# Performance work log

Hardware: AMD Instinct MI355X
Metric: run time of the kernel (lower is better)

Reference implementation:

```python
import jax, jax.numpy as jnp
import numpy as np

OUT_DIM = 64
NUM_HEADS = 8
HID = NUM_HEADS * OUT_DIM  # 512
ALPHA = 0.01  # leaky relu slope
N_NODES = 20000
N_EDGES = 100000
MP_LEN = 3


def setup_inputs() -> dict:
    key = jax.random.key(0)
    ks = jax.random.split(key, 8)
    s = 1.0 / np.sqrt(HID)
    return {
        "features": jax.random.normal(ks[0], (N_NODES, OUT_DIM), jnp.float32),
        "W_ih": jax.random.normal(ks[1], (3 * HID, OUT_DIM), jnp.float32) * s,
        "W_hh": jax.random.normal(ks[2], (3 * HID, HID), jnp.float32) * s,
        "b_ih": jax.random.normal(ks[3], (3 * HID,), jnp.float32) * s,
        "b_hh": jax.random.normal(ks[4], (3 * HID,), jnp.float32) * s,
        "attn": jax.random.normal(ks[5], (NUM_HEADS, OUT_DIM), jnp.float32) * 0.1,
        "edge_metapath_indices": jax.random.randint(ks[6], (N_EDGES, MP_LEN), 0, N_NODES),
        "edge_dst": jax.random.randint(ks[7], (N_EDGES,), 0, N_NODES),
    }


def _gru_last_hidden(x_seq, W_ih, W_hh, b_ih, b_hh):
    """x_seq: [L, E, D] -> final hidden [E, HID] (torch nn.GRU math, h0=0)."""
    E = x_seq.shape[1]
    h0 = jnp.zeros((E, HID), x_seq.dtype)

    def step(h, x):
        gi = x @ W_ih.T + b_ih  # [E, 3*HID]
        gh = h @ W_hh.T + b_hh  # [E, 3*HID]
        i_r, i_z, i_n = jnp.split(gi, 3, axis=-1)
        h_r, h_z, h_n = jnp.split(gh, 3, axis=-1)
        r = jax.nn.sigmoid(i_r + h_r)
        z = jax.nn.sigmoid(i_z + h_z)
        n = jnp.tanh(i_n + r * h_n)
        h_new = (1.0 - z) * n + z * h
        return h_new, None

    h_last, _ = jax.lax.scan(step, h0, x_seq)
    return h_last


def reference(features, W_ih, W_hh, b_ih, b_hh, attn,
              edge_metapath_indices, edge_dst):
    N = features.shape[0]
    # gather metapath node features: [E, L, D] -> GRU over L
    edata = features[edge_metapath_indices]
    h = _gru_last_hidden(jnp.transpose(edata, (1, 0, 2)), W_ih, W_hh, b_ih, b_hh)
    eft = h.reshape(-1, NUM_HEADS, OUT_DIM)  # [E, H, D]
    # attention logits per edge/head + leaky relu
    a = jnp.sum(eft * attn[None], axis=-1)  # [E, H]
    a = jnp.where(a >= 0, a, ALPHA * a)
    # edge softmax grouped by destination node
    amax = jax.ops.segment_max(a, edge_dst, num_segments=N)  # [N, H]
    ea = jnp.exp(a - amax[edge_dst])
    denom = jax.ops.segment_sum(ea, edge_dst, num_segments=N)  # [N, H]
    alpha = ea / denom[edge_dst]  # [E, H]
    # weighted message aggregation (sum) to destination nodes
    msg = eft * alpha[:, :, None]  # [E, H, D]
    ret = jax.ops.segment_sum(msg, edge_dst, num_segments=N)  # [N, H, D]
    return ret
```

## Files before the change

kernel.cpp:

```cpp
#include <hip/hip_runtime.h>
#include <hip/hip_bf16.h>

#define N_NODES 20000
#define N_EDGES 100000
#define HID 512
#define G3 1536
#define NH 8
#define OD 64

typedef __hip_bfloat16 bf16;
typedef __attribute__((ext_vector_type(8))) short bf16x8;
typedef __attribute__((ext_vector_type(4))) float f32x4;

__device__ __forceinline__ float fsig(float x) { return 1.0f / (1.0f + __expf(-x)); }
__device__ __forceinline__ float ftanh(float x) { return 1.0f - 2.0f / (__expf(2.0f * x) + 1.0f); }
__device__ __forceinline__ float b2f(bf16 b) { return __bfloat162float(b); }
__device__ __forceinline__ bf16 f2b(float f) { return __float2bfloat16(f); }
__device__ __forceinline__ float bs2f(short s) {
    return __uint_as_float(((unsigned)(unsigned short)s) << 16);
}
__device__ __forceinline__ float us2f(unsigned short s) {
    return __uint_as_float(((unsigned)s) << 16);
}
__device__ __forceinline__ short f2bs(float f) {
    bf16 b = __float2bfloat16(f);
    return *reinterpret_cast<short*>(&b);
}
__device__ __forceinline__ unsigned ford(float f) {
    unsigned u = __float_as_uint(f);
    return (u & 0x80000000u) ? ~u : (u | 0x80000000u);
}
__device__ __forceinline__ float iford(unsigned u) {
    return __uint_as_float((u & 0x80000000u) ? (u & 0x7fffffffu) : ~u);
}

__device__ __forceinline__ void g2l16(const void* g, void* l) {
#if __has_builtin(__builtin_amdgcn_global_load_lds)
    __builtin_amdgcn_global_load_lds((const __attribute__((address_space(1))) char*)g,
                                     (__attribute__((address_space(3))) char*)l, 16, 0, 0);
#else
    *(bf16x8*)l = *(const bf16x8*)g;
#endif
}


__global__ __launch_bounds__(256) void k_prep(const float* __restrict__ Whh,
                                              const float* __restrict__ Wih,
                                              bf16* __restrict__ WTs,
                                              float* __restrict__ WIT) {
    int t = blockIdx.x * 256 + threadIdx.x;
    if (t < 98304) {
        int T = t >> 10, c = (t >> 6) & 15, l = t & 63;
        int n = T * 16 + (l & 15);
        int k = c * 32 + ((l >> 4) << 3);
        const float* src = Whh + (size_t)n * 512 + k;
        bf16x8 v;
#pragma unroll
        for (int j = 0; j < 8; ++j) v[j] = f2bs(src[j]);
        *(bf16x8*)(WTs + (size_t)t * 8) = v;
    } else {
        int u = t - 98304;
        int d = u / 1536, j = u % 1536;
        WIT[u] = Wih[(size_t)j * 64 + d];
    }
}

__global__ __launch_bounds__(256) void k_count(const int* __restrict__ dst,
                                               unsigned* __restrict__ cnt) {
    int e = blockIdx.x * 256 + threadIdx.x;
    if (e < N_EDGES) atomicAdd(&cnt[dst[e]], 1u);
}

#define SCAN_CH 79
__global__ __launch_bounds__(256) void k_scan(const unsigned* __restrict__ cnt,
                                              unsigned* __restrict__ base,
                                              unsigned* __restrict__ cursor) {
    __shared__ unsigned ls[256];
    int t = threadIdx.x;
    int s0 = t * SCAN_CH;
    int s1 = s0 + SCAN_CH < N_NODES ? s0 + SCAN_CH : N_NODES;
    unsigned s = 0;
    for (int i = s0; i < s1; ++i) s += cnt[i];
    ls[t] = s;
    __syncthreads();
    for (int d = 1; d < 256; d <<= 1) {
        unsigned v = (t >= d) ? ls[t - d] : 0u;
        __syncthreads();
        ls[t] += v;
        __syncthreads();
    }
    unsigned run = ls[t] - s;
    for (int i = s0; i < s1; ++i) {
        base[i] = run; cursor[i] = run; run += cnt[i];
    }
    if (t == 255) base[N_NODES] = ls[255];
}

__global__ __launch_bounds__(256) void k_fill(const int* __restrict__ dst,
                                              unsigned* __restrict__ cursor,
                                              unsigned* __restrict__ csr) {
    int e = blockIdx.x * 256 + threadIdx.x;
    if (e < N_EDGES) {
        unsigned p = atomicAdd(&cursor[dst[e]], 1u);
        csr[p] = (unsigned)e;
    }
}

__global__ __launch_bounds__(256) void k_gi(const float* __restrict__ feat,
                                            const float* __restrict__ WIT,
                                            const float* __restrict__ b_ih,
                                            const float* __restrict__ b_hh,
                                            bf16* __restrict__ G,
                                            bf16* __restrict__ H1) {
    __shared__ float fs[16][64];
    const int n0 = blockIdx.x * 16;
    const int k = blockIdx.y * 256 + threadIdx.x;
    for (int i = threadIdx.x; i < 16 * 64; i += 256)
        fs[0][i] = feat[(size_t)n0 * 64 + i];
    __syncthreads();
    float acc[3][16];
#pragma unroll
    for (int g = 0; g < 3; ++g) {
        float b = b_ih[g * 512 + k];
#pragma unroll
        for (int e = 0; e < 16; ++e) acc[g][e] = b;
    }
    for (int d = 0; d < 64; d += 4) {
        float w[3][4];
#pragma unroll
        for (int u = 0; u < 4; ++u)
#pragma unroll
            for (int g = 0; g < 3; ++g)
                w[g][u] = WIT[(size_t)(d + u) * G3 + g * 512 + k];
#pragma unroll
        for (int e = 0; e < 16; ++e) {
            float4 f = *(const float4*)&fs[e][d];
#pragma unroll
            for (int g = 0; g < 3; ++g)
                acc[g][e] += w[g][0] * f.x + w[g][1] * f.y + w[g][2] * f.z + w[g][3] * f.w;
        }
    }
    const float br = b_hh[k], bz = b_hh[512 + k], bn = b_hh[1024 + k];
#pragma unroll
    for (int e = 0; e < 16; ++e) {
        bf16* dst = G + (size_t)(n0 + e) * G3 + k * 3;
        dst[0] = f2b(acc[0][e]);
        dst[1] = f2b(acc[1][e]);
        dst[2] = f2b(acc[2][e]);
        float r1 = fsig(acc[0][e] + br);
        float z1 = fsig(acc[1][e] + bz);
        float n1 = ftanh(acc[2][e] + r1 * bn);
        H1[(size_t)(n0 + e) * HID + k] = f2b((1.0f - z1) * n1);
    }
}

__global__ __launch_bounds__(256, 2) void k_gh2(const bf16* __restrict__ H1,
                                                const bf16* __restrict__ WTs,
                                                const float* __restrict__ b_hh,
                                                bf16* __restrict__ GH2) {
    __shared__ short Bs[3 * 8192];
    const int tid = threadIdx.x;
    const int wave = tid >> 6, lane = tid & 63;
    const int m0 = blockIdx.x * 128;
    const int k0 = (lane >> 4) << 3;

    bf16x8 afrag[2][16];
#pragma unroll
    for (int t = 0; t < 2; ++t) {
        int row = m0 + wave * 32 + t * 16 + (lane & 15);
        int ar = row < N_NODES ? row : N_NODES - 1;
#pragma unroll
        for (int c = 0; c < 16; ++c)
            afrag[t][c] = *(const bf16x8*)(H1 + (size_t)ar * HID + c * 32 + k0);
    }

    const bf16* wp[12];
    short* lp[12];
#pragma unroll
    for (int i = 0; i < 12; ++i) {
        int p = tid + i * 256;
        int g = p >> 10, q = p & 1023;
        wp[i] = WTs + (size_t)g * 32 * 8192 + q * 8;
        lp[i] = &Bs[g * 8192 + q * 8];
    }

    const int col = lane & 15;
    const int qb = (lane >> 4) << 2;
    for (int jt = 0; jt < 32; ++jt) {
        __syncthreads();
#pragma unroll
        for (int i = 0; i < 12; ++i) {
            g2l16(wp[i], lp[i]);
            wp[i] += 8192;
        }
        __syncthreads();
        f32x4 acc[2][3];
#pragma unroll
        for (int t = 0; t < 2; ++t)
#pragma unroll
            for (int g = 0; g < 3; ++g) acc[t][g] = (f32x4){0, 0, 0, 0};
        const int boff = lane * 8;
#pragma unroll
        for (int c = 0; c < 16; ++c) {
            bf16x8 b0 = *(const bf16x8*)&Bs[0 * 8192 + c * 512 + boff];
            bf16x8 b1 = *(const bf16x8*)&Bs[1 * 8192 + c * 512 + boff];
            bf16x8 b2 = *(const bf16x8*)&Bs[2 * 8192 + c * 512 + boff];
#pragma unroll
            for (int t = 0; t < 2; ++t) {
                acc[t][0] = __builtin_amdgcn_mfma_f32_16x16x32_bf16(afrag[t][c], b0, acc[t][0], 0, 0, 0);
                acc[t][1] = __builtin_amdgcn_mfma_f32_16x16x32_bf16(afrag[t][c], b1, acc[t][1], 0, 0, 0);
                acc[t][2] = __builtin_amdgcn_mfma_f32_16x16x32_bf16(afrag[t][c], b2, acc[t][2], 0, 0, 0);
            }
        }
        const int cj = jt * 16 + col;
        const float br = b_hh[cj], bz = b_hh[512 + cj], bn = b_hh[1024 + cj];
#pragma unroll
        for (int t = 0; t < 2; ++t)
#pragma unroll
            for (int q = 0; q < 4; ++q) {
                int e = m0 + wave * 32 + t * 16 + qb + q;
                if (e < N_NODES) {
                    bf16* dst = GH2 + (size_t)e * G3 + cj * 3;
                    dst[0] = f2b(acc[t][0][q] + br);
                    dst[1] = f2b(acc[t][1][q] + bz);
                    dst[2] = f2b(acc[t][2][q] + bn);
                }
            }
    }
}

__global__ __launch_bounds__(256) void k_h2(const bf16* __restrict__ G,
                                            const bf16* __restrict__ GH2,
                                            const bf16* __restrict__ H1,
                                            const int* __restrict__ emi,
                                            bf16* __restrict__ h2) {
    size_t i = (size_t)blockIdx.x * 256 + threadIdx.x;
    int e = (int)(i >> 6);
    int kc = (int)(i & 63) * 8;
    int i0 = emi[(size_t)e * 3 + 0];
    int i1 = emi[(size_t)e * 3 + 1];
    const bf16* g1p = G + (size_t)i1 * G3 + kc * 3;
    const bf16* ghp = GH2 + (size_t)i0 * G3 + kc * 3;
    bf16x8 h1v = *(const bf16x8*)(H1 + (size_t)i0 * HID + kc);
    short s1[24], sh[24];
    {
        bf16x8 a0 = *(const bf16x8*)g1p, a1 = *(const bf16x8*)(g1p + 8), a2 = *(const bf16x8*)(g1p + 16);
        bf16x8 c0 = *(const bf16x8*)ghp, c1 = *(const bf16x8*)(ghp + 8), c2 = *(const bf16x8*)(ghp + 16);
#pragma unroll
        for (int j = 0; j < 8; ++j) {
            s1[j] = a0[j]; s1[8 + j] = a1[j]; s1[16 + j] = a2[j];
            sh[j] = c0[j]; sh[8 + j] = c1[j]; sh[16 + j] = c2[j];
        }
    }
    bf16x8 out;
#pragma unroll
    for (int j = 0; j < 8; ++j) {
        float r = fsig(bs2f(s1[j * 3 + 0]) + bs2f(sh[j * 3 + 0]));
        float z = fsig(bs2f(s1[j * 3 + 1]) + bs2f(sh[j * 3 + 1]));
        float n = ftanh(bs2f(s1[j * 3 + 2]) + r * bs2f(sh[j * 3 + 2]));
        out[j] = f2bs((1.0f - z) * n + z * bs2f(h1v[j]));
    }
    *(bf16x8*)(h2 + (size_t)e * HID + kc) = out;
}

__global__ __launch_bounds__(256, 2) void k_gemm3(const bf16* __restrict__ G,
                                                  const bf16* __restrict__ WTs,
                                                  const float* __restrict__ b_hh,
                                                  const int* __restrict__ emi,
                                                  bf16* __restrict__ h2) {
    __shared__ short Bs[3 * 8192];
    __shared__ int si2[128];
    const int tid = threadIdx.x;
    const int wave = tid >> 6, lane = tid & 63;
    const int m0 = blockIdx.x * 128;
    if (tid < 128) {
        int e = m0 + tid;
        si2[tid] = emi[(size_t)(e < N_EDGES ? e : N_EDGES - 1) * 3 + 2];
    }
    const int k0 = (lane >> 4) << 3;

    bf16x8 afrag[2][16];
#pragma unroll
    for (int t = 0; t < 2; ++t) {
        int row = m0 + wave * 32 + t * 16 + (lane & 15);
        int ar = row < N_EDGES ? row : N_EDGES - 1;
#pragma unroll
        for (int c = 0; c < 16; ++c)
            afrag[t][c] = *(const bf16x8*)(h2 + (size_t)ar * HID + c * 32 + k0);
    }

    const bf16* wp[12];
    short* lp[12];
#pragma unroll
    for (int i = 0; i < 12; ++i) {
        int p = tid + i * 256;
        int g = p >> 10, q = p & 1023;
        wp[i] = WTs + (size_t)g * 32 * 8192 + q * 8;
        lp[i] = &Bs[g * 8192 + q * 8];
    }

    const int col = lane & 15;
    const int qb = (lane >> 4) << 2;
    for (int jt = 0; jt < 32; ++jt) {
        __syncthreads();
#pragma unroll
        for (int i = 0; i < 12; ++i) {
            g2l16(wp[i], lp[i]);
            wp[i] += 8192;
        }
        const int cj = jt * 16 + col;
        const float br = b_hh[cj], bz = b_hh[512 + cj], bn = b_hh[1024 + cj];
        unsigned short pg[2][4][3], ph[2][4];
#pragma unroll
        for (int t = 0; t < 2; ++t)
#pragma unroll
            for (int q = 0; q < 4; ++q) {
                int li = wave * 32 + t * 16 + qb + q;
                int e = m0 + li;
                int ec = e < N_EDGES ? e : N_EDGES - 1;
                const unsigned short* g2p =
                    (const unsigned short*)(G + (size_t)si2[li] * G3 + cj * 3);
                pg[t][q][0] = g2p[0]; pg[t][q][1] = g2p[1]; pg[t][q][2] = g2p[2];
                ph[t][q] = ((const unsigned short*)h2)[(size_t)ec * HID + cj];
            }
        __syncthreads();
        f32x4 acc[2][3];
#pragma unroll
        for (int t = 0; t < 2; ++t)
#pragma unroll
            for (int g = 0; g < 3; ++g) acc[t][g] = (f32x4){0, 0, 0, 0};
        const int boff = lane * 8;
#pragma unroll
        for (int c = 0; c < 16; ++c) {
            bf16x8 b0 = *(const bf16x8*)&Bs[0 * 8192 + c * 512 + boff];
            bf16x8 b1 = *(const bf16x8*)&Bs[1 * 8192 + c * 512 + boff];
            bf16x8 b2 = *(const bf16x8*)&Bs[2 * 8192 + c * 512 + boff];
#pragma unroll
            for (int t = 0; t < 2; ++t) {
                acc[t][0] = __builtin_amdgcn_mfma_f32_16x16x32_bf16(afrag[t][c], b0, acc[t][0], 0, 0, 0);
                acc[t][1] = __builtin_amdgcn_mfma_f32_16x16x32_bf16(afrag[t][c], b1, acc[t][1], 0, 0, 0);
                acc[t][2] = __builtin_amdgcn_mfma_f32_16x16x32_bf16(afrag[t][c], b2, acc[t][2], 0, 0, 0);
            }
        }
#pragma unroll
        for (int t = 0; t < 2; ++t)
#pragma unroll
            for (int q = 0; q < 4; ++q) {
                int e = m0 + wave * 32 + t * 16 + qb + q;
                if (e < N_EDGES) {
                    float r = fsig(us2f(pg[t][q][0]) + acc[t][0][q] + br);
                    float z = fsig(us2f(pg[t][q][1]) + acc[t][1][q] + bz);
                    float ng = ftanh(us2f(pg[t][q][2]) + r * (acc[t][2][q] + bn));
                    h2[(size_t)e * HID + cj] = f2b((1.0f - z) * ng + z * us2f(ph[t][q]));
                }
            }
    }
}

__global__ __launch_bounds__(256) void k_logits(const bf16* __restrict__ eft,
                                                const float* __restrict__ attn,
                                                const int* __restrict__ dst,
                                                float* __restrict__ a,
                                                unsigned* __restrict__ amax) {
    int i = blockIdx.x * 256 + threadIdx.x;
    int e = i >> 3, h = i & 7;
    const __hip_bfloat162* f2 = (const __hip_bfloat162*)(eft + (size_t)e * HID + h * OD);
    const float* at = attn + h * OD;
    float s = 0.f;
#pragma unroll
    for (int d = 0; d < OD / 2; ++d) {
        float2 fv = __bfloat1622float2(f2[d]);
        s += fv.x * at[2 * d] + fv.y * at[2 * d + 1];
    }
    s = (s >= 0.f) ? s : 0.01f * s;
    a[i] = s;
    atomicMax(&amax[(size_t)dst[e] * NH + h], ford(s));
}

__global__ __launch_bounds__(256) void k_ea(const int* __restrict__ dst,
                                            const unsigned* __restrict__ amax,
                                            float* __restrict__ a,
                                            float* __restrict__ denom) {
    int i = blockIdx.x * 256 + threadIdx.x;
    int e = i >> 3, h = i & 7;
    float m = iford(amax[(size_t)dst[e] * NH + h]);
    float v = __expf(a[i] - m);
    a[i] = v;
    atomicAdd(&denom[(size_t)dst[e] * NH + h], v);
}

__global__ __launch_bounds__(256) void k_out(const bf16* __restrict__ eft,
                                             const float* __restrict__ a,
                                             const float* __restrict__ denom,
                                             const unsigned* __restrict__ base,
                                             const unsigned* __restrict__ csr,
                                             float* __restrict__ out) {
    int n = blockIdx.x;
    int k = blockIdx.y * 256 + threadIdx.x;
    int h = k >> 6;
    unsigned b0 = base[n], b1 = base[n + 1];
    float rden = (b1 > b0) ? 1.0f / denom[(size_t)n * NH + h] : 0.0f;
    float acc = 0.f;
    for (unsigned i = b0; i < b1; ++i) {
        unsigned e = csr[i];
        float al = a[(size_t)e * NH + h];
        acc += b2f(eft[(size_t)e * HID + k]) * al;
    }
    out[(size_t)n * HID + k] = acc * rden;
}

extern "C" void kernel_launch(void* const* d_in, const int* in_sizes, int n_in,
                              void* d_out, int out_size, void* d_ws, size_t ws_size,
                              hipStream_t stream) {
    (void)in_sizes; (void)n_in; (void)ws_size; (void)out_size;
    const float* feat = (const float*)d_in[0];
    const float* W_ih = (const float*)d_in[1];
    const float* W_hh = (const float*)d_in[2];
    const float* b_ih = (const float*)d_in[3];
    const float* b_hh = (const float*)d_in[4];
    const float* attn = (const float*)d_in[5];
    const int* emi = (const int*)d_in[6];
    const int* dst = (const int*)d_in[7];
    float* out = (float*)d_out;

    char* ws = (char*)d_ws;
    bf16* G = (bf16*)ws;
    bf16* GH2 = (bf16*)(ws + 61440000);
    bf16* h2 = (bf16*)(ws + 122880000);
    bf16* WTs = (bf16*)(ws + 225280000);
    float* WIT = (float*)(ws + 226852864);
    float* a = (float*)(ws + 227246080);
    unsigned* amax = (unsigned*)(ws + 230446080);
    float* denom = (float*)(ws + 231086080);
    unsigned* cnt = (unsigned*)(ws + 231726080);
    unsigned* base = (unsigned*)(ws + 231806080);
    unsigned* cursor = (unsigned*)(ws + 231886088);
    unsigned* csr = (unsigned*)(ws + 231966088);
    bf16* H1 = (bf16*)(ws + 232366088);

    (void)hipMemsetAsync(amax, 0, 1360000, stream);

    k_prep<<<768, 256, 0, stream>>>(W_hh, W_ih, WTs, WIT);
    k_count<<<391, 256, 0, stream>>>(dst, cnt);
    k_scan<<<1, 256, 0, stream>>>(cnt, base, cursor);
    k_fill<<<391, 256, 0, stream>>>(dst, cursor, csr);
    k_gi<<<dim3(1250, 2), 256, 0, stream>>>(feat, WIT, b_ih, b_hh, G, H1);
    k_gh2<<<157, 256, 0, stream>>>(H1, WTs, b_hh, GH2);
    k_h2<<<25000, 256, 0, stream>>>(G, GH2, H1, emi, h2);
    k_gemm3<<<782, 256, 0, stream>>>(G, WTs, b_hh, emi, h2);
    k_logits<<<3125, 256, 0, stream>>>(h2, attn, dst, a, amax);
    k_ea<<<3125, 256, 0, stream>>>(dst, amax, a, denom);
    k_out<<<dim3(N_NODES, 2), 256, 0, stream>>>(h2, a, denom, base, csr, out);
}
```

Baseline: 863.0 us.

## Halve k_gemm3 row tile to 64 edges per block and use fast reciprocal

The GRU step-3 GEMM kernel now handles 64 edges per block instead of 128, with one 16-row MFMA tile per wave, and launches twice as many blocks. This lowers register pressure and spreads the work over more CUs, but each block still loads the full weight slab into shared memory, so global weight traffic per edge doubles. The sigmoid, tanh and softmax normalisation divisions are also replaced with the hardware approximate reciprocal, trading a little accuracy for fewer instructions.

```diff
diff --git a/kernel.cpp b/kernel.cpp
--- a/kernel.cpp
+++ b/kernel.cpp
@@ -12,8 +12,9 @@
 typedef __attribute__((ext_vector_type(8))) short bf16x8;
 typedef __attribute__((ext_vector_type(4))) float f32x4;
 
-__device__ __forceinline__ float fsig(float x) { return 1.0f / (1.0f + __expf(-x)); }
-__device__ __forceinline__ float ftanh(float x) { return 1.0f - 2.0f / (__expf(2.0f * x) + 1.0f); }
+__device__ __forceinline__ float frcp(float x) { return __builtin_amdgcn_rcpf(x); }
+__device__ __forceinline__ float fsig(float x) { return frcp(1.0f + __expf(-x)); }
+__device__ __forceinline__ float ftanh(float x) { return 1.0f - 2.0f * frcp(__expf(2.0f * x) + 1.0f); }
 __device__ __forceinline__ float b2f(bf16 b) { return __bfloat162float(b); }
 __device__ __forceinline__ bf16 f2b(float f) { return __float2bfloat16(f); }
 __device__ __forceinline__ float bs2f(short s) {
@@ -263,30 +264,29 @@
     *(bf16x8*)(h2 + (size_t)e * HID + kc) = out;
 }
 
-__global__ __launch_bounds__(256, 2) void k_gemm3(const bf16* __restrict__ G,
-                                                  const bf16* __restrict__ WTs,
-                                                  const float* __restrict__ b_hh,
-                                                  const int* __restrict__ emi,
-                                                  bf16* __restrict__ h2) {
+__global__ __launch_bounds__(256) void k_gemm3(const bf16* __restrict__ G,
+                                               const bf16* __restrict__ WTs,
+                                               const float* __restrict__ b_hh,
+                                               const int* __restrict__ emi,
+                                               bf16* __restrict__ h2) {
     __shared__ short Bs[3 * 8192];
-    __shared__ int si2[128];
+    __shared__ int si2[64];
     const int tid = threadIdx.x;
     const int wave = tid >> 6, lane = tid & 63;
-    const int m0 = blockIdx.x * 128;
-    if (tid < 128) {
+    const int m0 = blockIdx.x * 64;
+    if (tid < 64) {
         int e = m0 + tid;
         si2[tid] = emi[(size_t)(e < N_EDGES ? e : N_EDGES - 1) * 3 + 2];
     }
     const int k0 = (lane >> 4) << 3;
 
-    bf16x8 afrag[2][16];
-#pragma unroll
-    for (int t = 0; t < 2; ++t) {
-        int row = m0 + wave * 32 + t * 16 + (lane & 15);
+    bf16x8 afrag[16];
+    {
+        int row = m0 + wave * 16 + (lane & 15);
         int ar = row < N_EDGES ? row : N_EDGES - 1;
 #pragma unroll
         for (int c = 0; c < 16; ++c)
-            afrag[t][c] = *(const bf16x8*)(h2 + (size_t)ar * HID + c * 32 + k0);
+            afrag[c] = *(const bf16x8*)(h2 + (size_t)ar * HID + c * 32 + k0);
     }
 
     const bf16* wp[12];
@@ -310,50 +310,39 @@
         }
         const int cj = jt * 16 + col;
         const float br = b_hh[cj], bz = b_hh[512 + cj], bn = b_hh[1024 + cj];
-        unsigned short pg[2][4][3], ph[2][4];
-#pragma unroll
-        for (int t = 0; t < 2; ++t)
-#pragma unroll
-            for (int q = 0; q < 4; ++q) {
-                int li = wave * 32 + t * 16 + qb + q;
-                int e = m0 + li;
-                int ec = e < N_EDGES ? e : N_EDGES - 1;
-                const unsigned short* g2p =
-                    (const unsigned short*)(G + (size_t)si2[li] * G3 + cj * 3);
-                pg[t][q][0] = g2p[0]; pg[t][q][1] = g2p[1]; pg[t][q][2] = g2p[2];
-                ph[t][q] = ((const unsigned short*)h2)[(size_t)ec * HID + cj];
-            }
-        __syncthreads();
-        f32x4 acc[2][3];
-#pragma unroll
-        for (int t = 0; t < 2; ++t)
-#pragma unroll
-            for (int g = 0; g < 3; ++g) acc[t][g] = (f32x4){0, 0, 0, 0};
+        unsigned short pg[4][3], ph[4];
+#pragma unroll
+        for (int q = 0; q < 4; ++q) {
+            int li = wave * 16 + qb + q;
+            int e = m0 + li;
+            int ec = e < N_EDGES ? e : N_EDGES - 1;
+            const unsigned short* g2p =
+                (const unsigned short*)(G + (size_t)si2[li] * G3 + cj * 3);
+            pg[q][0] = g2p[0]; pg[q][1] = g2p[1]; pg[q][2] = g2p[2];
+            ph[q] = ((const unsigned short*)h2)[(size_t)ec * HID + cj];
+        }
+        __syncthreads();
+        f32x4 a0 = {0, 0, 0, 0}, a1 = {0, 0, 0, 0}, a2 = {0, 0, 0, 0};
         const int boff = lane * 8;
 #pragma unroll
         for (int c = 0; c < 16; ++c) {
             bf16x8 b0 = *(const bf16x8*)&Bs[0 * 8192 + c * 512 + boff];
             bf16x8 b1 = *(const bf16x8*)&Bs[1 * 8192 + c * 512 + boff];
             bf16x8 b2 = *(const bf16x8*)&Bs[2 * 8192 + c * 512 + boff];
-#pragma unroll
-            for (int t = 0; t < 2; ++t) {
-                acc[t][0] = __builtin_amdgcn_mfma_f32_16x16x32_bf16(afrag[t][c], b0, acc[t][0], 0, 0, 0);
-                acc[t][1] = __builtin_amdgcn_mfma_f32_16x16x32_bf16(afrag[t][c], b1, acc[t][1], 0, 0, 0);
-                acc[t][2] = __builtin_amdgcn_mfma_f32_16x16x32_bf16(afrag[t][c], b2, acc[t][2], 0, 0, 0);
+            a0 = __builtin_amdgcn_mfma_f32_16x16x32_bf16(afrag[c], b0, a0, 0, 0, 0);
+            a1 = __builtin_amdgcn_mfma_f32_16x16x32_bf16(afrag[c], b1, a1, 0, 0, 0);
+            a2 = __builtin_amdgcn_mfma_f32_16x16x32_bf16(afrag[c], b2, a2, 0, 0, 0);
+        }
+#pragma unroll
+        for (int q = 0; q < 4; ++q) {
+            int e = m0 + wave * 16 + qb + q;
+            if (e < N_EDGES) {
+                float r = fsig(us2f(pg[q][0]) + a0[q] + br);
+                float z = fsig(us2f(pg[q][1]) + a1[q] + bz);
+                float ng = ftanh(us2f(pg[q][2]) + r * (a2[q] + bn));
+                h2[(size_t)e * HID + cj] = f2b((1.0f - z) * ng + z * us2f(ph[q]));
             }
         }
-#pragma unroll
-        for (int t = 0; t < 2; ++t)
-#pragma unroll
-            for (int q = 0; q < 4; ++q) {
-                int e = m0 + wave * 32 + t * 16 + qb + q;
-                if (e < N_EDGES) {
-                    float r = fsig(us2f(pg[t][q][0]) + acc[t][0][q] + br);
-                    float z = fsig(us2f(pg[t][q][1]) + acc[t][1][q] + bz);
-                    float ng = ftanh(us2f(pg[t][q][2]) + r * (acc[t][2][q] + bn));
-                    h2[(size_t)e * HID + cj] = f2b((1.0f - z) * ng + z * us2f(ph[t][q]));
-                }
-            }
     }
 }
 
@@ -399,7 +388,7 @@
     int k = blockIdx.y * 256 + threadIdx.x;
     int h = k >> 6;
     unsigned b0 = base[n], b1 = base[n + 1];
-    float rden = (b1 > b0) ? 1.0f / denom[(size_t)n * NH + h] : 0.0f;
+    float rden = (b1 > b0) ? frcp(denom[(size_t)n * NH + h]) : 0.0f;
     float acc = 0.f;
     for (unsigned i = b0; i < b1; ++i) {
         unsigned e = csr[i];
@@ -447,7 +436,7 @@
     k_gi<<<dim3(1250, 2), 256, 0, stream>>>(feat, WIT, b_ih, b_hh, G, H1);
     k_gh2<<<157, 256, 0, stream>>>(H1, WTs, b_hh, GH2);
     k_h2<<<25000, 256, 0, stream>>>(G, GH2, H1, emi, h2);
-    k_gemm3<<<782, 256, 0, stream>>>(G, WTs, b_hh, emi, h2);
+    k_gemm3<<<1563, 256, 0, stream>>>(G, WTs, b_hh, emi, h2);
     k_logits<<<3125, 256, 0, stream>>>(h2, attn, dst, a, amax);
     k_ea<<<3125, 256, 0, stream>>>(dst, amax, a, denom);
     k_out<<<dim3(N_NODES, 2), 256, 0, stream>>>(h2, a, denom, base, csr, out);
```

New measurement: 804.8 us. 1.07x faster.
